# Kernel tuning notes

Hardware: AMD Instinct MI355X
Metric: run time of the kernel (lower is better)

## Reference

```python
import jax, jax.numpy as jnp
import numpy as np

EPS = 1e-5      # BatchNorm eps (torch default)
SLOPE = 0.2     # LeakyReLU negative slope


def _ico_conv(x, neigh, W, b):
    """Spherical 1-ring conv: gather K=7 neighbors per vertex, then linear.
    x: (B, C, V) float; neigh: (V, K) int; W: (O, C*K); b: (O,) -> (B, O, V).
    """
    B, C, V = x.shape
    K = neigh.shape[1]
    g = x[:, :, neigh]                             # (B, C, V, K) gather
    g = g.transpose(0, 2, 1, 3).reshape(B, V, C * K)  # per-vertex patch, C-major
    return jnp.einsum('bvi,oi->bov', g, W) + b[None, :, None]


def _bn_lrelu(x, gamma, beta):
    """BatchNorm1d (batch stats only, track_running_stats=False) + LeakyReLU(0.2).
    x: (B, C, V); normalize each channel over (B, V) with biased variance.
    """
    mean = x.mean(axis=(0, 2), keepdims=True)
    var = x.var(axis=(0, 2), keepdims=True)
    y = (x - mean) * jax.lax.rsqrt(var + EPS)
    y = y * gamma[None, :, None] + beta[None, :, None]
    return jnp.where(y >= 0, y, SLOPE * y)


def setup_inputs() -> dict:
    key = jax.random.key(0)
    ks = jax.random.split(key, 8)
    B, IN_CH, OUT_CH = 16, 32, 64
    N_FINE, N_COARSE, K = 163842, 40962, 7   # ico order 7 -> order 6
    x = jax.random.normal(ks[0], (B, IN_CH, N_FINE), dtype=jnp.float32)
    down_neigh_indices = jax.random.randint(ks[1], (N_COARSE, K), 0, N_FINE)
    conv_neigh_indices = jax.random.randint(ks[2], (N_COARSE, K), 0, N_COARSE)
    s1 = 1.0 / np.sqrt(IN_CH * K)
    s2 = 1.0 / np.sqrt(OUT_CH * K)
    w1 = jax.random.uniform(ks[3], (OUT_CH, IN_CH * K), minval=-s1, maxval=s1, dtype=jnp.float32)
    b1 = jax.random.uniform(ks[4], (OUT_CH,), minval=-s1, maxval=s1, dtype=jnp.float32)
    w2 = jax.random.uniform(ks[5], (OUT_CH, OUT_CH * K), minval=-s2, maxval=s2, dtype=jnp.float32)
    b2 = jax.random.uniform(ks[6], (OUT_CH,), minval=-s2, maxval=s2, dtype=jnp.float32)
    g1 = jnp.ones((OUT_CH,), jnp.float32)
    beta1 = jnp.zeros((OUT_CH,), jnp.float32)
    g2 = jnp.ones((OUT_CH,), jnp.float32)
    beta2 = jnp.zeros((OUT_CH,), jnp.float32)
    return dict(x=x, w1=w1, b1=b1, g1=g1, beta1=beta1, w2=w2, b2=b2, g2=g2,
                beta2=beta2, conv_neigh_indices=conv_neigh_indices,
                down_neigh_indices=down_neigh_indices)


def reference(x, w1, b1, g1, beta1, w2, b2, g2, beta2,
              conv_neigh_indices, down_neigh_indices):
    # IcoPoolLayer, mean mode: gather 7 fine-mesh neighbors per coarse vertex,
    # average over the neighborhood. (B, C, N_fine) -> (B, C, N_coarse)
    xp = x[:, :, down_neigh_indices].mean(axis=-1)
    # (conv -> BN -> LeakyReLU) x 2 at the coarse sampling
    h = _bn_lrelu(_ico_conv(xp, conv_neigh_indices, w1, b1), g1, beta1)
    h = _bn_lrelu(_ico_conv(h, conv_neigh_indices, w2, b2), g2, beta2)
    return h  # max_pool_indices is None for mean pooling
```

## Files before the change

### kernel.cpp

```cpp
#include <hip/hip_runtime.h>
#include <hip/hip_bf16.h>


#define B_SZ     16
#define CIN      32
#define CMID     64
#define VFINE    163842
#define VC       40962
#define KNB      7

typedef __attribute__((ext_vector_type(8))) short  short8;
typedef __attribute__((ext_vector_type(4))) float  f32x4;
typedef __attribute__((ext_vector_type(4))) unsigned short u16x4;

__device__ inline float bf2f(unsigned short u) {
    return __builtin_bit_cast(float, (unsigned int)(((unsigned int)u) << 16));
}
__device__ inline unsigned short f2bf(float f) {
    __hip_bfloat16 h = __float2bfloat16(f);
    return __builtin_bit_cast(unsigned short, h);
}

__global__ void prep_w(const float* __restrict__ w1, const float* __restrict__ w2,
                       unsigned short* __restrict__ w1f, unsigned short* __restrict__ w2f,
                       float* __restrict__ stats) {
    int tid = blockIdx.x * blockDim.x + threadIdx.x;
    int stride = gridDim.x * blockDim.x;
    if (blockIdx.x == 0 && threadIdx.x < 256) stats[threadIdx.x] = 0.f;
    const int total1 = 7 * 4 * 64 * 8;
    for (int idx = tid; idx < total1; idx += stride) {
        int j = idx & 7, l = (idx >> 3) & 63, t = (idx >> 9) & 3, cc = idx >> 11;
        int o = t * 16 + (l & 15);
        int kk = (l >> 4) * 8 + j;
        w1f[idx] = f2bf(w1[o * 224 + kk * 7 + cc]);
    }
    const int total2 = 14 * 4 * 64 * 8;
    for (int idx = tid; idx < total2; idx += stride) {
        int j = idx & 7, l = (idx >> 3) & 63, t = (idx >> 9) & 3, cc = idx >> 11;
        int o = t * 16 + (l & 15);
        int kk = (l >> 4) * 8 + j;
        int k = cc >> 1, ch = cc & 1;
        int c = ch * 32 + kk;
        w2f[idx] = f2bf(w2[o * 448 + c * 7 + k]);
    }
}

__global__ __launch_bounds__(256) void transpose_x(const float* __restrict__ x,
                                                   unsigned short* __restrict__ xt, int vf) {
    __shared__ __align__(16) unsigned short lds[64 * 258];
    const int t = threadIdx.x;
    const int v0 = blockIdx.x * 64;
    const int j  = t & 15;
    const int r0 = t >> 4;
    const int lane = t & 63;
    const int wid = t >> 6;

#pragma unroll
    for (int p = 0; p < 2; ++p) {
        if (p) __syncthreads();
#pragma unroll
        for (int it = 0; it < 16; ++it) {
            int r = r0 + it * 16;
            int row = p * 256 + r;
            int vg = v0 + 4 * j;
            f32x4 d = {0.f, 0.f, 0.f, 0.f};
            if (vg + 3 < vf) {
                d = *reinterpret_cast<const f32x4*>(x + (size_t)row * vf + vg);
            } else {
#pragma unroll
                for (int q = 0; q < 4; ++q)
                    if (vg + q < vf) d[q] = x[(size_t)row * vf + vg + q];
            }
#pragma unroll
            for (int q = 0; q < 4; ++q)
                lds[(4 * j + q) * 258 + r] = f2bf(d[q]);
        }
        __syncthreads();
#pragma unroll
        for (int i = 0; i < 16; ++i) {
            int v = wid * 16 + i;
            u16x4 o = *reinterpret_cast<const u16x4*>(lds + v * 258 + 4 * lane);
            if (v0 + v < vf)
                *reinterpret_cast<u16x4*>(xt + (size_t)(v0 + v) * 512 + p * 256 + 4 * lane) = o;
        }
    }
}

__global__ __launch_bounds__(256) void pool_k(const unsigned short* __restrict__ xt,
                                              const int* __restrict__ dn,
                                              unsigned short* __restrict__ xp, int vc) {
    int wid = (blockIdx.x * blockDim.x + threadIdx.x) >> 6;
    int lane = threadIdx.x & 63;
    if (wid >= vc) return;
    float acc[8];
#pragma unroll
    for (int j = 0; j < 8; ++j) acc[j] = 0.f;
#pragma unroll
    for (int k = 0; k < 7; ++k) {
        int n = dn[(size_t)wid * 7 + k];
        short8 d = *reinterpret_cast<const short8*>(xt + (size_t)n * 512 + lane * 8);
#pragma unroll
        for (int j = 0; j < 8; ++j) acc[j] += bf2f((unsigned short)d[j]);
    }
    short8 o;
#pragma unroll
    for (int j = 0; j < 8; ++j) o[j] = (short)f2bf(acc[j] * (1.f / 7.f));
    *reinterpret_cast<short8*>(xp + (size_t)wid * 512 + lane * 8) = o;
}

template <int CCH, bool BN_IN>
__global__ __launch_bounds__(256) void conv_mfma(const unsigned short* __restrict__ xin,
                                                 const int* __restrict__ neigh,
                                                 const unsigned short* __restrict__ wfrag,
                                                 const float* __restrict__ bnp,
                                                 unsigned short* __restrict__ hout,
                                                 float* __restrict__ stats,
                                                 int vc, int ngroups) {
    constexpr int C = 32 * CCH;
    constexpr int NCHUNK = 7 * CCH;
    __shared__ __align__(16) unsigned short wlds[NCHUNK * 4 * 64 * 8];
    __shared__ float bsum[128];
    for (int i = threadIdx.x; i < NCHUNK * 256; i += 256)
        reinterpret_cast<short8*>(wlds)[i] = reinterpret_cast<const short8*>(wfrag)[i];
    if (threadIdx.x < 128) bsum[threadIdx.x] = 0.f;
    __syncthreads();

    const int wid = threadIdx.x >> 6;
    const int lane = threadIdx.x & 63;
    const int lb = lane & 15, lg = lane >> 4;

    float scv[CCH][8], shv[CCH][8];
    if constexpr (BN_IN) {
#pragma unroll
        for (int ch = 0; ch < CCH; ++ch)
#pragma unroll
            for (int j = 0; j < 8; ++j) {
                scv[ch][j] = bnp[ch * 32 + lg * 8 + j];
                shv[ch][j] = bnp[64 + ch * 32 + lg * 8 + j];
            }
    }

    float ssum[16], ssq[16];
#pragma unroll
    for (int i = 0; i < 16; ++i) { ssum[i] = 0.f; ssq[i] = 0.f; }

    for (int grp = blockIdx.x; grp < ngroups; grp += gridDim.x) {
        const int v0 = grp * 16 + wid * 4;
        f32x4 acc[4][4];
#pragma unroll
        for (int i = 0; i < 4; ++i)
#pragma unroll
            for (int t = 0; t < 4; ++t) acc[i][t] = (f32x4){0.f, 0.f, 0.f, 0.f};

        auto do_k = [&](int k) {
            int n[4];
#pragma unroll
            for (int i = 0; i < 4; ++i) {
                int v = v0 + i;
                n[i] = (v < vc) ? neigh[(size_t)v * 7 + k] : 0;
            }
#pragma unroll
            for (int ch = 0; ch < CCH; ++ch) {
                const int chunk = k * CCH + ch;
                const short8* wp = reinterpret_cast<const short8*>(wlds) + (chunk * 4) * 64 + lane;
                short8 a0 = wp[0];
                short8 a1 = wp[64];
                short8 a2 = wp[128];
                short8 a3 = wp[192];
#pragma unroll
                for (int i = 0; i < 4; ++i) {
                    short8 b = *reinterpret_cast<const short8*>(
                        xin + (size_t)n[i] * (16 * C) + lb * C + ch * 32 + lg * 8);
                    if constexpr (BN_IN) {
                        short8 bb;
#pragma unroll
                        for (int j = 0; j < 8; ++j) {
                            float z = fmaf(scv[ch][j], bf2f((unsigned short)b[j]), shv[ch][j]);
                            z = fmaxf(z, 0.2f * z);
                            bb[j] = (short)f2bf(z);
                        }
                        b = bb;
                    }
                    acc[i][0] = __builtin_amdgcn_mfma_f32_16x16x32_bf16(a0, b, acc[i][0], 0, 0, 0);
                    acc[i][1] = __builtin_amdgcn_mfma_f32_16x16x32_bf16(a1, b, acc[i][1], 0, 0, 0);
                    acc[i][2] = __builtin_amdgcn_mfma_f32_16x16x32_bf16(a2, b, acc[i][2], 0, 0, 0);
                    acc[i][3] = __builtin_amdgcn_mfma_f32_16x16x32_bf16(a3, b, acc[i][3], 0, 0, 0);
                }
            }
        };
        if constexpr (BN_IN) {
#pragma unroll 2
            for (int k = 0; k < 7; ++k) do_k(k);
        } else {
#pragma unroll 1
            for (int k = 0; k < 7; ++k) do_k(k);
        }

#pragma unroll
        for (int i = 0; i < 4; ++i) {
            const int v = v0 + i;
            if (v < vc) {
#pragma unroll
                for (int t = 0; t < 4; ++t) {
                    u16x4 st;
#pragma unroll
                    for (int r = 0; r < 4; ++r) {
                        float f = acc[i][t][r];
                        ssum[t * 4 + r] += f;
                        ssq[t * 4 + r] += f * f;
                        st[r] = f2bf(f);
                    }
                    *reinterpret_cast<u16x4*>(hout + (size_t)v * 1024 + lb * 64 + t * 16 + lg * 4) = st;
                }
            }
        }
    }
#pragma unroll
    for (int m = 1; m <= 8; m <<= 1) {
#pragma unroll
        for (int i = 0; i < 16; ++i) {
            ssum[i] += __shfl_xor(ssum[i], m, 64);
            ssq[i] += __shfl_xor(ssq[i], m, 64);
        }
    }
    if (lb == 0) {
#pragma unroll
        for (int t = 0; t < 4; ++t)
#pragma unroll
            for (int r = 0; r < 4; ++r) {
                int o = t * 16 + lg * 4 + r;
                atomicAdd(&bsum[o], ssum[t * 4 + r]);
                atomicAdd(&bsum[64 + o], ssq[t * 4 + r]);
            }
    }
    __syncthreads();
    if (threadIdx.x < 128) atomicAdd(&stats[threadIdx.x], bsum[threadIdx.x]);
}

__global__ void bn_params(const float* __restrict__ stats, const float* __restrict__ gamma,
                          const float* __restrict__ beta, float* __restrict__ params, float inv_n) {
    int o = threadIdx.x;
    if (o < 64) {
        float mean = stats[o] * inv_n;
        float var = stats[64 + o] * inv_n - mean * mean;
        float sc = gamma[o] * rsqrtf(var + 1e-5f);
        params[o] = sc;
        params[64 + o] = beta[o] - mean * sc;
    }
}

__global__ __launch_bounds__(256) void final_out(const unsigned short* __restrict__ h2,
                                                 const float* __restrict__ params,
                                                 float* __restrict__ out, int vc) {
    __shared__ float lds[128 * 65];
    const int t = threadIdx.x;
    const int v0 = blockIdx.x * 64;
    const int sub = t & 15, vloc = t >> 4;
    const int o0 = (sub & 7) * 8;
    float sc[8], sh[8];
#pragma unroll
    for (int j = 0; j < 8; ++j) { sc[j] = params[o0 + j]; sh[j] = params[64 + o0 + j]; }
    for (int c = 0; c < 8; ++c) {
        if (c) __syncthreads();
#pragma unroll
        for (int i = 0; i < 4; ++i) {
            int v = v0 + vloc + 16 * i;
            short8 d = {0, 0, 0, 0, 0, 0, 0, 0};
            if (v < vc)
                d = *reinterpret_cast<const short8*>(h2 + (size_t)v * 1024 + c * 128 + sub * 8);
#pragma unroll
            for (int j = 0; j < 8; ++j) {
                float y = sc[j] * bf2f((unsigned short)d[j]) + sh[j];
                y = fmaxf(y, 0.2f * y);
                lds[(sub * 8 + j) * 65 + vloc + 16 * i] = y;
            }
        }
        __syncthreads();
#pragma unroll
        for (int q = 0; q < 8; ++q) {
            int idx = t + 256 * q;
            int r = idx >> 4;
            int vq = (idx & 15) * 4;
            int v = v0 + vq;
            const float* lp = lds + r * 65 + vq;
            if (v + 3 < vc) {
                f32x4 o = {lp[0], lp[1], lp[2], lp[3]};
                *reinterpret_cast<f32x4*>(out + (size_t)(c * 128 + r) * vc + v) = o;
            } else {
#pragma unroll
                for (int e = 0; e < 4; ++e)
                    if (v + e < vc) out[(size_t)(c * 128 + r) * vc + v + e] = lp[e];
            }
        }
    }
}

extern "C" void kernel_launch(void* const* d_in, const int* in_sizes, int n_in,
                              void* d_out, int out_size, void* d_ws, size_t ws_size,
                              hipStream_t stream) {
    const float* x   = (const float*)d_in[0];
    const float* w1  = (const float*)d_in[1];
    const float* g1  = (const float*)d_in[3];
    const float* be1 = (const float*)d_in[4];
    const float* w2  = (const float*)d_in[5];
    const float* g2  = (const float*)d_in[7];
    const float* be2 = (const float*)d_in[8];
    const int* cn    = (const int*)d_in[9];
    const int* dn    = (const int*)d_in[10];
    float* out = (float*)d_out;

    char* ws = (char*)d_ws;
    size_t off = 0;
    auto take = [&](size_t bytes) { size_t o = off; off = (off + bytes + 255) & ~(size_t)255; return o; };
    unsigned short* xp  = (unsigned short*)(ws + take((size_t)VC * 512 * 2));
    unsigned short* h1  = (unsigned short*)(ws + take((size_t)VC * 1024 * 2));
    unsigned short* h2  = (unsigned short*)(ws + take((size_t)VC * 1024 * 2));
    unsigned short* w1f = (unsigned short*)(ws + take(7 * 4 * 64 * 8 * 2));
    unsigned short* w2f = (unsigned short*)(ws + take(14 * 4 * 64 * 8 * 2));
    float* stats        = (float*)(ws + take(256 * 4));
    float* params       = (float*)(ws + take(256 * 4));

    unsigned short* xt = (unsigned short*)d_out;

    const float inv_n = 1.0f / (16.0f * (float)VC);
    const int ngroups = (VC + 15) / 16;

    prep_w<<<32, 256, 0, stream>>>(w1, w2, w1f, w2f, stats);
    transpose_x<<<(VFINE + 63) / 64, 256, 0, stream>>>(x, xt, VFINE);
    pool_k<<<(VC + 3) / 4, 256, 0, stream>>>(xt, dn, xp, VC);
    conv_mfma<1, false><<<512, 256, 0, stream>>>(xp, cn, w1f, nullptr, h1, stats, VC, ngroups);
    bn_params<<<1, 64, 0, stream>>>(stats, g1, be1, params, inv_n);
    conv_mfma<2, true><<<512, 256, 0, stream>>>(h1, cn, w2f, params, h2, stats + 128, VC, ngroups);
    bn_params<<<1, 64, 0, stream>>>(stats + 128, g2, be2, params + 128, inv_n);
    final_out<<<(VC + 63) / 64, 256, 0, stream>>>(h2, params + 128, out, VC);
}
```

Before: 587.6 us.

## Split BN stats and BN apply out of conv into separate streaming kernels

Removes the fused per-element BN+LeakyReLU from the second conv's gather path and the stats reduction from the conv epilogue. Adds standalone stats_k and bn_apply kernels that stream h1/h2 linearly. Conv now uses one 512-thread block per 32 vertices instead of a persistent grid. This trades redundant 7x BN recomputation on gathered neighbors for extra full passes over the activation buffers. Stats are now computed from bf16-rounded values, which changes numerics slightly.

```diff
diff --git a/kernel.cpp b/kernel.cpp
--- a/kernel.cpp
+++ b/kernel.cpp
@@ -108,130 +108,108 @@
     *reinterpret_cast<short8*>(xp + (size_t)wid * 512 + lane * 8) = o;
 }
 
-template <int CCH, bool BN_IN>
-__global__ __launch_bounds__(256) void conv_mfma(const unsigned short* __restrict__ xin,
-                                                 const int* __restrict__ neigh,
-                                                 const unsigned short* __restrict__ wfrag,
-                                                 const float* __restrict__ bnp,
-                                                 unsigned short* __restrict__ hout,
-                                                 float* __restrict__ stats,
-                                                 int vc, int ngroups) {
+template <int CCH>
+__global__ __launch_bounds__(512, 4) void conv_mfma(const unsigned short* __restrict__ xin,
+                                                    const int* __restrict__ neigh,
+                                                    const unsigned short* __restrict__ wfrag,
+                                                    unsigned short* __restrict__ hout,
+                                                    int vc) {
     constexpr int C = 32 * CCH;
     constexpr int NCHUNK = 7 * CCH;
-    __shared__ __align__(16) unsigned short wlds[NCHUNK * 4 * 64 * 8];
-    __shared__ float bsum[128];
-    for (int i = threadIdx.x; i < NCHUNK * 256; i += 256)
+    __shared__ __align__(16) unsigned short wlds[NCHUNK * 2048];
+    for (int i = threadIdx.x; i < NCHUNK * 256; i += 512)
         reinterpret_cast<short8*>(wlds)[i] = reinterpret_cast<const short8*>(wfrag)[i];
-    if (threadIdx.x < 128) bsum[threadIdx.x] = 0.f;
     __syncthreads();
 
     const int wid = threadIdx.x >> 6;
     const int lane = threadIdx.x & 63;
     const int lb = lane & 15, lg = lane >> 4;
-
-    float scv[CCH][8], shv[CCH][8];
-    if constexpr (BN_IN) {
-#pragma unroll
-        for (int ch = 0; ch < CCH; ++ch)
-#pragma unroll
-            for (int j = 0; j < 8; ++j) {
-                scv[ch][j] = bnp[ch * 32 + lg * 8 + j];
-                shv[ch][j] = bnp[64 + ch * 32 + lg * 8 + j];
-            }
-    }
-
-    float ssum[16], ssq[16];
-#pragma unroll
-    for (int i = 0; i < 16; ++i) { ssum[i] = 0.f; ssq[i] = 0.f; }
-
-    for (int grp = blockIdx.x; grp < ngroups; grp += gridDim.x) {
-        const int v0 = grp * 16 + wid * 4;
-        f32x4 acc[4][4];
-#pragma unroll
-        for (int i = 0; i < 4; ++i)
-#pragma unroll
-            for (int t = 0; t < 4; ++t) acc[i][t] = (f32x4){0.f, 0.f, 0.f, 0.f};
-
-        auto do_k = [&](int k) {
-            int n[4];
+    const int v0 = blockIdx.x * 32 + wid * 4;
+    const int boff = lb * C + lg * 8;
+
+    f32x4 acc[4][4];
+#pragma unroll
+    for (int i = 0; i < 4; ++i)
+#pragma unroll
+        for (int t = 0; t < 4; ++t) acc[i][t] = (f32x4){0.f, 0.f, 0.f, 0.f};
+
+#pragma unroll 1
+    for (int k = 0; k < 7; ++k) {
+        int n[4];
+#pragma unroll
+        for (int i = 0; i < 4; ++i) {
+            int v = v0 + i;
+            n[i] = (v < vc) ? neigh[(size_t)v * 7 + k] : 0;
+        }
+#pragma unroll
+        for (int ch = 0; ch < CCH; ++ch) {
+            const int chunk = k * CCH + ch;
+            const short8* wp = reinterpret_cast<const short8*>(wlds) + (chunk * 4) * 64 + lane;
+            short8 a0 = wp[0];
+            short8 a1 = wp[64];
+            short8 a2 = wp[128];
+            short8 a3 = wp[192];
 #pragma unroll
             for (int i = 0; i < 4; ++i) {
-                int v = v0 + i;
-                n[i] = (v < vc) ? neigh[(size_t)v * 7 + k] : 0;
-            }
-#pragma unroll
-            for (int ch = 0; ch < CCH; ++ch) {
-                const int chunk = k * CCH + ch;
-                const short8* wp = reinterpret_cast<const short8*>(wlds) + (chunk * 4) * 64 + lane;
-                short8 a0 = wp[0];
-                short8 a1 = wp[64];
-                short8 a2 = wp[128];
-                short8 a3 = wp[192];
-#pragma unroll
-                for (int i = 0; i < 4; ++i) {
-                    short8 b = *reinterpret_cast<const short8*>(
-                        xin + (size_t)n[i] * (16 * C) + lb * C + ch * 32 + lg * 8);
-                    if constexpr (BN_IN) {
-                        short8 bb;
-#pragma unroll
-                        for (int j = 0; j < 8; ++j) {
-                            float z = fmaf(scv[ch][j], bf2f((unsigned short)b[j]), shv[ch][j]);
-                            z = fmaxf(z, 0.2f * z);
-                            bb[j] = (short)f2bf(z);
-                        }
-                        b = bb;
-                    }
-                    acc[i][0] = __builtin_amdgcn_mfma_f32_16x16x32_bf16(a0, b, acc[i][0], 0, 0, 0);
-                    acc[i][1] = __builtin_amdgcn_mfma_f32_16x16x32_bf16(a1, b, acc[i][1], 0, 0, 0);
-                    acc[i][2] = __builtin_amdgcn_mfma_f32_16x16x32_bf16(a2, b, acc[i][2], 0, 0, 0);
-                    acc[i][3] = __builtin_amdgcn_mfma_f32_16x16x32_bf16(a3, b, acc[i][3], 0, 0, 0);
-                }
-            }
-        };
-        if constexpr (BN_IN) {
-#pragma unroll 2
-            for (int k = 0; k < 7; ++k) do_k(k);
-        } else {
-#pragma unroll 1
-            for (int k = 0; k < 7; ++k) do_k(k);
-        }
-
-#pragma unroll
-        for (int i = 0; i < 4; ++i) {
-            const int v = v0 + i;
-            if (v < vc) {
-#pragma unroll
-                for (int t = 0; t < 4; ++t) {
-                    u16x4 st;
-#pragma unroll
-                    for (int r = 0; r < 4; ++r) {
-                        float f = acc[i][t][r];
-                        ssum[t * 4 + r] += f;
-                        ssq[t * 4 + r] += f * f;
-                        st[r] = f2bf(f);
-                    }
-                    *reinterpret_cast<u16x4*>(hout + (size_t)v * 1024 + lb * 64 + t * 16 + lg * 4) = st;
-                }
-            }
-        }
-    }
-#pragma unroll
-    for (int m = 1; m <= 8; m <<= 1) {
-#pragma unroll
-        for (int i = 0; i < 16; ++i) {
-            ssum[i] += __shfl_xor(ssum[i], m, 64);
-            ssq[i] += __shfl_xor(ssq[i], m, 64);
-        }
-    }
-    if (lb == 0) {
-#pragma unroll
-        for (int t = 0; t < 4; ++t)
-#pragma unroll
-            for (int r = 0; r < 4; ++r) {
-                int o = t * 16 + lg * 4 + r;
-                atomicAdd(&bsum[o], ssum[t * 4 + r]);
-                atomicAdd(&bsum[64 + o], ssq[t * 4 + r]);
-            }
+                const short8 b = *reinterpret_cast<const short8*>(
+                    xin + (size_t)n[i] * (16 * C) + boff + ch * 32);
+                acc[i][0] = __builtin_amdgcn_mfma_f32_16x16x32_bf16(a0, b, acc[i][0], 0, 0, 0);
+                acc[i][1] = __builtin_amdgcn_mfma_f32_16x16x32_bf16(a1, b, acc[i][1], 0, 0, 0);
+                acc[i][2] = __builtin_amdgcn_mfma_f32_16x16x32_bf16(a2, b, acc[i][2], 0, 0, 0);
+                acc[i][3] = __builtin_amdgcn_mfma_f32_16x16x32_bf16(a3, b, acc[i][3], 0, 0, 0);
+            }
+        }
+    }
+#pragma unroll
+    for (int i = 0; i < 4; ++i) {
+        const int v = v0 + i;
+        if (v < vc) {
+#pragma unroll
+            for (int t = 0; t < 4; ++t) {
+                u16x4 st;
+#pragma unroll
+                for (int r = 0; r < 4; ++r) st[r] = f2bf(acc[i][t][r]);
+                *reinterpret_cast<u16x4*>(hout + (size_t)v * 1024 + lb * 64 + t * 16 + lg * 4) = st;
+            }
+        }
+    }
+}
+
+__global__ __launch_bounds__(256) void stats_k(const unsigned short* __restrict__ h,
+                                               float* __restrict__ stats, int total8) {
+    __shared__ float bsum[128];
+    if (threadIdx.x < 128) bsum[threadIdx.x] = 0.f;
+    __syncthreads();
+    const int lane = threadIdx.x & 63;
+    int idx0 = blockIdx.x * blockDim.x + threadIdx.x;
+    int stride = gridDim.x * blockDim.x;
+    const int c0 = (idx0 & 7) * 8;
+    float s[8], q[8];
+#pragma unroll
+    for (int j = 0; j < 8; ++j) { s[j] = 0.f; q[j] = 0.f; }
+    for (int idx = idx0; idx < total8; idx += stride) {
+        short8 d = *reinterpret_cast<const short8*>(h + (size_t)idx * 8);
+#pragma unroll
+        for (int j = 0; j < 8; ++j) {
+            float f = bf2f((unsigned short)d[j]);
+            s[j] += f;
+            q[j] += f * f;
+        }
+    }
+#pragma unroll
+    for (int m = 8; m <= 32; m <<= 1) {
+#pragma unroll
+        for (int j = 0; j < 8; ++j) {
+            s[j] += __shfl_xor(s[j], m, 64);
+            q[j] += __shfl_xor(q[j], m, 64);
+        }
+    }
+    if (lane < 8) {
+#pragma unroll
+        for (int j = 0; j < 8; ++j) {
+            atomicAdd(&bsum[c0 + j], s[j]);
+            atomicAdd(&bsum[64 + c0 + j], q[j]);
+        }
     }
     __syncthreads();
     if (threadIdx.x < 128) atomicAdd(&stats[threadIdx.x], bsum[threadIdx.x]);
@@ -246,6 +224,27 @@
         float sc = gamma[o] * rsqrtf(var + 1e-5f);
         params[o] = sc;
         params[64 + o] = beta[o] - mean * sc;
+    }
+}
+
+__global__ __launch_bounds__(256) void bn_apply(unsigned short* __restrict__ h,
+                                                const float* __restrict__ params, int total8) {
+    int stride = gridDim.x * blockDim.x;
+    int idx0 = blockIdx.x * blockDim.x + threadIdx.x;
+    int c0 = (idx0 & 7) * 8;
+    float sc[8], sh[8];
+#pragma unroll
+    for (int j = 0; j < 8; ++j) { sc[j] = params[c0 + j]; sh[j] = params[64 + c0 + j]; }
+    for (int idx = idx0; idx < total8; idx += stride) {
+        short8 d = *reinterpret_cast<const short8*>(h + (size_t)idx * 8);
+        short8 o;
+#pragma unroll
+        for (int j = 0; j < 8; ++j) {
+            float y = sc[j] * bf2f((unsigned short)d[j]) + sh[j];
+            y = fmaxf(y, 0.2f * y);
+            o[j] = (short)f2bf(y);
+        }
+        *reinterpret_cast<short8*>(h + (size_t)idx * 8) = o;
     }
 }
 
@@ -323,14 +322,17 @@
     unsigned short* xt = (unsigned short*)d_out;
 
     const float inv_n = 1.0f / (16.0f * (float)VC);
-    const int ngroups = (VC + 15) / 16;
+    const int nblk2 = (VC + 31) / 32;
 
     prep_w<<<32, 256, 0, stream>>>(w1, w2, w1f, w2f, stats);
     transpose_x<<<(VFINE + 63) / 64, 256, 0, stream>>>(x, xt, VFINE);
     pool_k<<<(VC + 3) / 4, 256, 0, stream>>>(xt, dn, xp, VC);
-    conv_mfma<1, false><<<512, 256, 0, stream>>>(xp, cn, w1f, nullptr, h1, stats, VC, ngroups);
+    conv_mfma<1><<<nblk2, 512, 0, stream>>>(xp, cn, w1f, h1, VC);
+    stats_k<<<2048, 256, 0, stream>>>(h1, stats, VC * 128);
     bn_params<<<1, 64, 0, stream>>>(stats, g1, be1, params, inv_n);
-    conv_mfma<2, true><<<512, 256, 0, stream>>>(h1, cn, w2f, params, h2, stats + 128, VC, ngroups);
+    bn_apply<<<2048, 256, 0, stream>>>(h1, params, VC * 128);
+    conv_mfma<2><<<nblk2, 512, 0, stream>>>(h1, cn, w2f, h2, VC);
+    stats_k<<<2048, 256, 0, stream>>>(h2, stats + 128, VC * 128);
     bn_params<<<1, 64, 0, stream>>>(stats + 128, g2, be2, params + 128, inv_n);
     final_out<<<(VC + 63) / 64, 256, 0, stream>>>(h2, params + 128, out, VC);
 }
```

Measured after the change: 570.3 us. 2.9% less time.
